# Kernel tuning notes

Measured on AMD Instinct MI355X. Metric: run time of the kernel, lower is better.

## Reference

```python
import jax, jax.numpy as jnp
import numpy as np

N_NODES = 50000
N_EDGES = 800000
IN_DIM = 128
HID_DIM = 128
N_CLASSES = 2


def setup_inputs() -> dict:
    key = jax.random.key(0)
    ks = jax.random.split(key, 8)
    glorot = lambda k, shp: jax.random.normal(k, shp, dtype=jnp.float32) * (2.0 / (shp[0] + shp[1])) ** 0.5
    return {
        "x": jax.random.normal(ks[0], (N_NODES, IN_DIM), dtype=jnp.float32),
        "edge_index": jax.random.randint(ks[1], (2, N_EDGES), 0, N_NODES, dtype=jnp.int64),
        "W1": glorot(ks[2], (IN_DIM, HID_DIM)),
        "b1": jnp.zeros((HID_DIM,), dtype=jnp.float32),
        "W2": glorot(ks[3], (HID_DIM, HID_DIM)),
        "b2": jnp.zeros((HID_DIM,), dtype=jnp.float32),
        "Wc": glorot(ks[4], (HID_DIM, N_CLASSES)),
        "bc": jnp.zeros((N_CLASSES,), dtype=jnp.float32),
    }


def _gcn_norm(edge_index, num_nodes):
    # PyG gcn_norm with self-loops: norm_e = deg[src]^-1/2 * deg[dst]^-1/2
    loop = jnp.arange(num_nodes, dtype=edge_index.dtype)
    src = jnp.concatenate([edge_index[0], loop])
    dst = jnp.concatenate([edge_index[1], loop])
    deg = jax.ops.segment_sum(jnp.ones_like(dst, dtype=jnp.float32), dst,
                              num_segments=num_nodes)
    dis = jnp.where(deg > 0, jax.lax.rsqrt(jnp.maximum(deg, 1.0)), 0.0)
    norm = dis[src] * dis[dst]  # [E + N]
    return src, dst, norm


def _gcn_conv(h, src, dst, norm, W, b, num_nodes):
    h = h @ W                              # [N, out]
    msg = h[src] * norm[:, None]           # gather + scale  [E+N, out]
    out = jax.ops.segment_sum(msg, dst, num_segments=num_nodes)  # scatter-add
    return out + b


def reference(x, edge_index, W1, b1, W2, b2, Wc, bc):
    n = x.shape[0]
    src, dst, norm = _gcn_norm(edge_index, n)
    h = _gcn_conv(x, src, dst, norm, W1, b1, n)
    h = jax.nn.relu(h)  # dropout is identity in eval mode
    h = _gcn_conv(h, src, dst, norm, W2, b2, n)
    return h @ Wc + bc  # [N, num_classes]
```

## Files before the change

### kernel.cpp

```cpp
#include <hip/hip_runtime.h>

static inline size_t align_up(size_t x, size_t a) { return (x + a - 1) & ~(a - 1); }

typedef short bf16x8 __attribute__((ext_vector_type(8)));
typedef float f32x4 __attribute__((ext_vector_type(4)));
typedef int i32x4 __attribute__((ext_vector_type(4)));
typedef float f32x4v __attribute__((ext_vector_type(4)));
typedef unsigned u32x4 __attribute__((ext_vector_type(4)));

#define BK 64
#define SEGE 4096
#define CAP 32
#define PAD 64

__device__ __forceinline__ unsigned bf_rne(float x) {
  unsigned u = __float_as_uint(x);
  return (u + 0x7FFFu + ((u >> 16) & 1u)) >> 16;
}
__device__ __forceinline__ unsigned bf_pack(float lo, float hi) {
  return bf_rne(lo) | (bf_rne(hi) << 16);
}

union BFU { u32x4 u; bf16x8 v; };


__global__ __launch_bounds__(256) void k1_kernel(const int* __restrict__ ei, int E,
                                                 int nseg, int nb,
                                                 unsigned* __restrict__ queue,
                                                 int* __restrict__ hdr,
                                                 const float* __restrict__ W1,
                                                 const float* __restrict__ W2,
                                                 const float* __restrict__ Wc,
                                                 const float* __restrict__ b2,
                                                 const float* __restrict__ bc,
                                                 u32x4* __restrict__ Bpack,
                                                 float* __restrict__ Wf,
                                                 float* __restrict__ bf) {
  __shared__ int lcnt[832];
  __shared__ float sWc[256];
  int t = threadIdx.x;
  int b = blockIdx.x;
  if (b < nseg) {
    for (int i = t; i < nb; i += 256) lcnt[i] = 0;
    __syncthreads();
#pragma unroll
    for (int j = 0; j < SEGE / 1024; ++j) {
      int e = b * SEGE + j * 1024 + t * 4;
      if (e < E) {
        i32x4 s4 = __builtin_nontemporal_load((const i32x4*)(ei + e));
        i32x4 d4 = __builtin_nontemporal_load((const i32x4*)(ei + E + e));
        int ss[4] = {s4.x, s4.y, s4.z, s4.w};
        int dd[4] = {d4.x, d4.y, d4.z, d4.w};
#pragma unroll
        for (int k = 0; k < 4; ++k) {
          int bkt = dd[k] >> 6;
          int off = atomicAdd(&lcnt[bkt], 1);
          if (off < CAP)
            queue[((size_t)bkt * nseg + b) * CAP + off] =
                (unsigned)ss[k] | ((unsigned)(dd[k] & 63) << 16);
        }
      }
    }
    __syncthreads();
    for (int i = t; i < nb; i += 256) hdr[(size_t)b * nb + i] = min(lcnt[i], CAP);
  } else if (b < nseg + 8) {
    int idx = (b - nseg) * 256 + t;
    int l = idx & 63;
    int s = (idx >> 6) & 3;
    int ct = idx >> 8;
    int k0 = s * 32 + (l >> 4) * 8;
    int col = ct * 16 + (l & 15);
    float v[8];
#pragma unroll
    for (int j = 0; j < 8; ++j) v[j] = W1[(size_t)(k0 + j) * 128 + col];
    u32x4 u;
    u.x = bf_pack(v[0], v[1]);
    u.y = bf_pack(v[2], v[3]);
    u.z = bf_pack(v[4], v[5]);
    u.w = bf_pack(v[6], v[7]);
    Bpack[idx] = u;
  } else {
    sWc[t] = Wc[t];
    __syncthreads();
    int i = t >> 1, c = t & 1;
    const float4* row = (const float4*)(W2 + (size_t)i * 128);
    float s = 0.f;
#pragma unroll
    for (int k4 = 0; k4 < 32; ++k4) {
      float4 w = row[k4];
      s = fmaf(w.x, sWc[(k4 * 4 + 0) * 2 + c], s);
      s = fmaf(w.y, sWc[(k4 * 4 + 1) * 2 + c], s);
      s = fmaf(w.z, sWc[(k4 * 4 + 2) * 2 + c], s);
      s = fmaf(w.w, sWc[(k4 * 4 + 3) * 2 + c], s);
    }
    Wf[i * 2 + c] = s;
    if (i == 0) {
      float bb = bc[c];
      for (int k = 0; k < 128; ++k) bb = fmaf(b2[k], sWc[k * 2 + c], bb);
      bf[c] = bb;
    }
  }
}


__global__ __launch_bounds__(256) void k2_kernel(const unsigned* __restrict__ queue,
                                                 const int* __restrict__ hdr,
                                                 int nseg, int nb,
                                                 int* __restrict__ cnt,
                                                 unsigned short* __restrict__ csr_src,
                                                 int n_nodes,
                                                 const float* __restrict__ x,
                                                 const u32x4* __restrict__ Bpack,
                                                 unsigned short* __restrict__ hout,
                                                 int n_rows) {
  __shared__ float sT[4][16][66];
  int t = threadIdx.x;
  if ((int)blockIdx.x < nb) {
    unsigned short* scsr = (unsigned short*)sT;
    int* ccur = (int*)((char*)sT + BK * PAD * 2);
    int* hdrL = ccur + BK;
    int bk = blockIdx.x;
    if (t < BK) ccur[t] = 0;
    if (t < nseg) hdrL[t] = hdr[(size_t)t * nb + bk];
    __syncthreads();
    const unsigned* qbk = queue + (size_t)bk * nseg * CAP;
    int slots = nseg * CAP;
    for (int sl = t; sl < slots; sl += 256) {
      int seg = sl >> 5;
      int off = sl & (CAP - 1);
      if (off < hdrL[seg]) {
        unsigned u = qbk[sl];
        int dl = (u >> 16) & 63;
        int p = atomicAdd(&ccur[dl], 1);
        if (p < PAD) scsr[dl * PAD + p] = (unsigned short)(u & 0xFFFFu);
      }
    }
    __syncthreads();
    uint4* gdst = (uint4*)(csr_src + (size_t)bk * BK * PAD);
    const uint4* lsrc = (const uint4*)scsr;
    gdst[t] = lsrc[t];
    gdst[t + 256] = lsrc[t + 256];
    if (t < BK) {
      int gn = bk * BK + t;
      if (gn < n_nodes) cnt[gn] = min(ccur[t], PAD);
    }
    return;
  }
  int w = t >> 6, l = t & 63;
  int rowbase = ((int)blockIdx.x - nb) * 64 + w * 16;
  int r = l & 15, kg = l >> 4;
  int grow = rowbase + r;
  bool valid = grow < n_rows;
  const float* xr = x + (size_t)grow * 128;

  bf16x8 afrag[4];
#pragma unroll
  for (int s = 0; s < 4; ++s) {
    f32x4v lo = {0.f, 0.f, 0.f, 0.f}, hi = lo;
    if (valid) {
      lo = __builtin_nontemporal_load((const f32x4v*)(xr + s * 32 + kg * 8));
      hi = __builtin_nontemporal_load((const f32x4v*)(xr + s * 32 + kg * 8 + 4));
    }
    BFU bu;
    bu.u.x = bf_pack(lo.x, lo.y);
    bu.u.y = bf_pack(lo.z, lo.w);
    bu.u.z = bf_pack(hi.x, hi.y);
    bu.u.w = bf_pack(hi.z, hi.w);
    afrag[s] = bu.v;
  }

  f32x4 acc[8] = {};
  const u32x4* bp = Bpack + l;
  u32x4 b0[4], b1[4];
#pragma unroll
  for (int s = 0; s < 4; ++s) b0[s] = bp[s * 64];

#define MM_STEP(CT, CUR, NXT)                                                   \
  {                                                                             \
    if (CT < 7) {                                                               \
      _Pragma("unroll") for (int s = 0; s < 4; ++s) NXT[s] =                    \
          bp[((CT + 1) * 4 + s) * 64];                                          \
    }                                                                           \
    _Pragma("unroll") for (int s = 0; s < 4; ++s) {                             \
      BFU bb;                                                                   \
      bb.u = CUR[s];                                                            \
      acc[CT] = __builtin_amdgcn_mfma_f32_16x16x32_bf16(afrag[s], bb.v,         \
                                                        acc[CT], 0, 0, 0);      \
    }                                                                           \
  }
  MM_STEP(0, b0, b1)
  MM_STEP(1, b1, b0)
  MM_STEP(2, b0, b1)
  MM_STEP(3, b1, b0)
  MM_STEP(4, b0, b1)
  MM_STEP(5, b1, b0)
  MM_STEP(6, b0, b1)
  MM_STEP(7, b1, b0)
#undef MM_STEP

  int erow = l >> 2;
  int eseg = l & 3;
  int g2 = rowbase + erow;
#pragma unroll
  for (int hf = 0; hf < 2; ++hf) {
    __syncthreads();
#pragma unroll
    for (int ct = 0; ct < 4; ++ct) {
#pragma unroll
      for (int rg = 0; rg < 4; ++rg)
        sT[w][kg * 4 + rg][ct * 16 + r] = acc[hf * 4 + ct][rg];
    }
    __syncthreads();
    float4 v0 = *(const float4*)&sT[w][erow][eseg * 16 + 0];
    float4 v1 = *(const float4*)&sT[w][erow][eseg * 16 + 4];
    float4 v2 = *(const float4*)&sT[w][erow][eseg * 16 + 8];
    float4 v3 = *(const float4*)&sT[w][erow][eseg * 16 + 12];
    if (g2 < n_rows) {
      u32x4 ua, ub;
      ua.x = bf_pack(v0.x, v0.y);
      ua.y = bf_pack(v0.z, v0.w);
      ua.z = bf_pack(v1.x, v1.y);
      ua.w = bf_pack(v1.z, v1.w);
      ub.x = bf_pack(v2.x, v2.y);
      ub.y = bf_pack(v2.z, v2.w);
      ub.z = bf_pack(v3.x, v3.y);
      ub.w = bf_pack(v3.z, v3.w);
      u32x4* dst = (u32x4*)(hout + (size_t)g2 * 128 + hf * 64 + eseg * 16);
      __builtin_nontemporal_store(ua, dst);
      __builtin_nontemporal_store(ub, dst + 1);
    }
  }
}


__global__ __launch_bounds__(256) void agg1_kernel(const unsigned short* __restrict__ h,
                                                   const unsigned short* __restrict__ csr_src,
                                                   const int* __restrict__ cnt,
                                                   const float* __restrict__ bias,
                                                   const float* __restrict__ Wf,
                                                   float2* __restrict__ g_out,
                                                   int n_nodes) {
  int node = blockIdx.x * 4 + (threadIdx.x >> 6);
  if (node >= n_nodes) return;
  int lane = threadIdx.x & 63;
  int g = lane >> 4;
  int sub = lane & 15;
  int deg = cnt[node];
  if (deg > PAD) deg = PAD;
  float dn = rsqrtf((float)(cnt[node] + 1));
  float a[8] = {};
#define UNPACK_FMA8(u, s)                                                  \
  {                                                                        \
    a[0] = fmaf(s, __uint_as_float((u).x << 16), a[0]);                    \
    a[1] = fmaf(s, __uint_as_float((u).x & 0xFFFF0000u), a[1]);            \
    a[2] = fmaf(s, __uint_as_float((u).y << 16), a[2]);                    \
    a[3] = fmaf(s, __uint_as_float((u).y & 0xFFFF0000u), a[3]);            \
    a[4] = fmaf(s, __uint_as_float((u).z << 16), a[4]);                    \
    a[5] = fmaf(s, __uint_as_float((u).z & 0xFFFF0000u), a[5]);            \
    a[6] = fmaf(s, __uint_as_float((u).w << 16), a[6]);                    \
    a[7] = fmaf(s, __uint_as_float((u).w & 0xFFFF0000u), a[7]);            \
  }
  if (g == 0) {
    uint4 su = ((const uint4*)(h + (size_t)node * 128))[sub];
    UNPACK_FMA8(su, dn);
  }
  const unsigned short* crow = csr_src + (size_t)node * PAD;
  int s_my = 0;
  float w_my = 0.f;
  if (lane < deg) {
    s_my = crow[lane];
    w_my = rsqrtf((float)(cnt[s_my] + 1));
  }
  for (int t0 = 0; t0 < deg; t0 += 16) {
    int t = t0 + g;
    int s0 = __shfl(s_my, t, 64);       float y0 = __shfl(w_my, t, 64);
    int s1 = __shfl(s_my, t + 4, 64);   float y1 = __shfl(w_my, t + 4, 64);
    int s2 = __shfl(s_my, t + 8, 64);   float y2 = __shfl(w_my, t + 8, 64);
    int s3 = __shfl(s_my, t + 12, 64);  float y3 = __shfl(w_my, t + 12, 64);
    uint4 u0 = ((const uint4*)(h + (size_t)s0 * 128))[sub];
    uint4 u1 = ((const uint4*)(h + (size_t)s1 * 128))[sub];
    uint4 u2 = ((const uint4*)(h + (size_t)s2 * 128))[sub];
    uint4 u3 = ((const uint4*)(h + (size_t)s3 * 128))[sub];
    UNPACK_FMA8(u0, y0);
    UNPACK_FMA8(u1, y1);
    UNPACK_FMA8(u2, y2);
    UNPACK_FMA8(u3, y3);
  }
#pragma unroll
  for (int c = 0; c < 8; ++c) {
    a[c] += __shfl_xor(a[c], 16, 64);
    a[c] += __shfl_xor(a[c], 32, 64);
  }
  const float4* b4 = (const float4*)bias;
  float4 bb0 = b4[sub * 2], bb1 = b4[sub * 2 + 1];
  float o[8];
  o[0] = fmaxf(fmaf(a[0], dn, bb0.x), 0.f);
  o[1] = fmaxf(fmaf(a[1], dn, bb0.y), 0.f);
  o[2] = fmaxf(fmaf(a[2], dn, bb0.z), 0.f);
  o[3] = fmaxf(fmaf(a[3], dn, bb0.w), 0.f);
  o[4] = fmaxf(fmaf(a[4], dn, bb1.x), 0.f);
  o[5] = fmaxf(fmaf(a[5], dn, bb1.y), 0.f);
  o[6] = fmaxf(fmaf(a[6], dn, bb1.z), 0.f);
  o[7] = fmaxf(fmaf(a[7], dn, bb1.w), 0.f);
  const float2* wf2 = (const float2*)Wf;
  int kbase = sub * 8;
  float p0 = 0.f, p1 = 0.f;
#pragma unroll
  for (int j = 0; j < 8; ++j) {
    float2 w = wf2[kbase + j];
    p0 = fmaf(o[j], w.x, p0);
    p1 = fmaf(o[j], w.y, p1);
  }
#pragma unroll
  for (int off = 8; off; off >>= 1) {
    p0 += __shfl_xor(p0, off, 64);
    p1 += __shfl_xor(p1, off, 64);
  }
  if (lane == 0) g_out[node] = make_float2(p0, p1);
}


__global__ __launch_bounds__(256) void agg2_kernel(const float2* __restrict__ gin,
                                                   const unsigned short* __restrict__ csr_src,
                                                   const int* __restrict__ cnt,
                                                   const float* __restrict__ bf,
                                                   float2* __restrict__ out, int n_nodes) {
  int tid = threadIdx.x;
  int node = blockIdx.x * 32 + (tid >> 3);
  if (node >= n_nodes) return;
  int sl = tid & 7;
  float dn = rsqrtf((float)(cnt[node] + 1));
  float2 acc = make_float2(0.f, 0.f);
  if (sl == 0) {
    float2 gs = gin[node];
    acc.x = dn * gs.x;
    acc.y = dn * gs.y;
  }
  int deg = cnt[node];
  if (deg > PAD) deg = PAD;
  const unsigned short* crow = csr_src + (size_t)node * PAD;
  for (int e = sl; e < deg; e += 8) {
    int s = crow[e];
    float w = rsqrtf((float)(cnt[s] + 1));
    float2 gv = gin[s];
    acc.x = fmaf(w, gv.x, acc.x);
    acc.y = fmaf(w, gv.y, acc.y);
  }
#pragma unroll
  for (int off = 1; off < 8; off <<= 1) {
    acc.x += __shfl_xor(acc.x, off, 64);
    acc.y += __shfl_xor(acc.y, off, 64);
  }
  if (sl == 0) {
    float2 o;
    o.x = fmaf(acc.x, dn, bf[0]);
    o.y = fmaf(acc.y, dn, bf[1]);
    out[node] = o;
  }
}


extern "C" void kernel_launch(void* const* d_in, const int* in_sizes, int n_in,
                              void* d_out, int out_size, void* d_ws, size_t ws_size,
                              hipStream_t stream) {
  const float* x  = (const float*)d_in[0];
  const int*   ei = (const int*)d_in[1];
  const float* W1 = (const float*)d_in[2];
  const float* b1 = (const float*)d_in[3];
  const float* W2 = (const float*)d_in[4];
  const float* b2 = (const float*)d_in[5];
  const float* Wc = (const float*)d_in[6];
  const float* bc = (const float*)d_in[7];
  float* out = (float*)d_out;

  int N = in_sizes[0] / 128;
  int E = in_sizes[1] / 2;

  int nseg = (E + SEGE - 1) / SEGE;
  int nb   = (N + BK - 1) / BK;

  char* p = (char*)d_ws;
  size_t o = 0;
  auto alloc = [&](size_t bytes) {
    void* r = p + o;
    o = align_up(o + bytes, 256);
    return r;
  };
  unsigned* queue = (unsigned*)alloc((size_t)nb * nseg * CAP * 4);
  int*      hdr   = (int*)alloc((size_t)nseg * nb * 4);
  int*      cnt   = (int*)alloc((size_t)N * 4);
  unsigned short* csr_src = (unsigned short*)alloc((size_t)nb * BK * PAD * 2);
  unsigned short* hBF = (unsigned short*)alloc((size_t)N * 128 * 2);
  float2*   gbuf  = (float2*)alloc((size_t)N * 8);
  u32x4*    Bpack = (u32x4*)alloc(2048 * 16);
  float*    Wf    = (float*)alloc(128 * 2 * 4);
  float*    bf    = (float*)alloc(2 * 4);
  (void)ws_size;

  int nmm = (N + 63) / 64;

  k1_kernel<<<nseg + 9, 256, 0, stream>>>(ei, E, nseg, nb, queue, hdr,
                                          W1, W2, Wc, b2, bc, Bpack, Wf, bf);
  k2_kernel<<<nb + nmm, 256, 0, stream>>>(queue, hdr, nseg, nb, cnt, csr_src, N,
                                          x, Bpack, hBF, N);
  agg1_kernel<<<(N + 3) / 4, 256, 0, stream>>>(hBF, csr_src, cnt, b1, Wf, gbuf, N);
  agg2_kernel<<<(N + 31) / 32, 256, 0, stream>>>(gbuf, csr_src, cnt, (const float*)bf,
                                                 (float2*)out, N);
}
```

Baseline: 80.45 us.

## Split binning into 1024-thread kernel and reorder k2 blocks matmul-first

The weight-prep work moves out of the fused k1 kernel into its own small kprep kernel. Edge binning goes into a separate kbin kernel where each 1024-thread block handles one 4096-edge segment in a single pass instead of four loop iterations of 256 threads. In k2 the block order is swapped so the matmul blocks come first and the CSR-build blocks come last. The goal is more parallelism during binning and better scheduling overlap in k2, at the cost of one extra kernel launch.

```diff
diff --git a/kernel.cpp b/kernel.cpp
--- a/kernel.cpp
+++ b/kernel.cpp
@@ -24,47 +24,19 @@
 union BFU { u32x4 u; bf16x8 v; };
 
 
-__global__ __launch_bounds__(256) void k1_kernel(const int* __restrict__ ei, int E,
-                                                 int nseg, int nb,
-                                                 unsigned* __restrict__ queue,
-                                                 int* __restrict__ hdr,
-                                                 const float* __restrict__ W1,
-                                                 const float* __restrict__ W2,
-                                                 const float* __restrict__ Wc,
-                                                 const float* __restrict__ b2,
-                                                 const float* __restrict__ bc,
-                                                 u32x4* __restrict__ Bpack,
-                                                 float* __restrict__ Wf,
-                                                 float* __restrict__ bf) {
-  __shared__ int lcnt[832];
+__global__ __launch_bounds__(256) void kprep_kernel(const float* __restrict__ W1,
+                                                    const float* __restrict__ W2,
+                                                    const float* __restrict__ Wc,
+                                                    const float* __restrict__ b2,
+                                                    const float* __restrict__ bc,
+                                                    u32x4* __restrict__ Bpack,
+                                                    float* __restrict__ Wf,
+                                                    float* __restrict__ bf) {
   __shared__ float sWc[256];
   int t = threadIdx.x;
   int b = blockIdx.x;
-  if (b < nseg) {
-    for (int i = t; i < nb; i += 256) lcnt[i] = 0;
-    __syncthreads();
-#pragma unroll
-    for (int j = 0; j < SEGE / 1024; ++j) {
-      int e = b * SEGE + j * 1024 + t * 4;
-      if (e < E) {
-        i32x4 s4 = __builtin_nontemporal_load((const i32x4*)(ei + e));
-        i32x4 d4 = __builtin_nontemporal_load((const i32x4*)(ei + E + e));
-        int ss[4] = {s4.x, s4.y, s4.z, s4.w};
-        int dd[4] = {d4.x, d4.y, d4.z, d4.w};
-#pragma unroll
-        for (int k = 0; k < 4; ++k) {
-          int bkt = dd[k] >> 6;
-          int off = atomicAdd(&lcnt[bkt], 1);
-          if (off < CAP)
-            queue[((size_t)bkt * nseg + b) * CAP + off] =
-                (unsigned)ss[k] | ((unsigned)(dd[k] & 63) << 16);
-        }
-      }
-    }
-    __syncthreads();
-    for (int i = t; i < nb; i += 256) hdr[(size_t)b * nb + i] = min(lcnt[i], CAP);
-  } else if (b < nseg + 8) {
-    int idx = (b - nseg) * 256 + t;
+  if (b < 8) {
+    int idx = b * 256 + t;
     int l = idx & 63;
     int s = (idx >> 6) & 3;
     int ct = idx >> 8;
@@ -103,9 +75,38 @@
 }
 
 
+__global__ __launch_bounds__(1024) void kbin_kernel(const int* __restrict__ ei, int E,
+                                                    int nseg, int nb,
+                                                    unsigned* __restrict__ queue,
+                                                    int* __restrict__ hdr) {
+  __shared__ int lcnt[832];
+  int t = threadIdx.x;
+  int b = blockIdx.x;
+  for (int i = t; i < nb; i += 1024) lcnt[i] = 0;
+  __syncthreads();
+  int e = b * SEGE + t * 4;
+  if (e < E) {
+    i32x4 s4 = __builtin_nontemporal_load((const i32x4*)(ei + e));
+    i32x4 d4 = __builtin_nontemporal_load((const i32x4*)(ei + E + e));
+    int ss[4] = {s4.x, s4.y, s4.z, s4.w};
+    int dd[4] = {d4.x, d4.y, d4.z, d4.w};
+#pragma unroll
+    for (int k = 0; k < 4; ++k) {
+      int bkt = dd[k] >> 6;
+      int off = atomicAdd(&lcnt[bkt], 1);
+      if (off < CAP)
+        queue[((size_t)bkt * nseg + b) * CAP + off] =
+            (unsigned)ss[k] | ((unsigned)(dd[k] & 63) << 16);
+    }
+  }
+  __syncthreads();
+  for (int i = t; i < nb; i += 1024) hdr[(size_t)b * nb + i] = min(lcnt[i], CAP);
+}
+
+
 __global__ __launch_bounds__(256) void k2_kernel(const unsigned* __restrict__ queue,
                                                  const int* __restrict__ hdr,
-                                                 int nseg, int nb,
+                                                 int nseg, int nb, int nmm,
                                                  int* __restrict__ cnt,
                                                  unsigned short* __restrict__ csr_src,
                                                  int n_nodes,
@@ -115,11 +116,11 @@
                                                  int n_rows) {
   __shared__ float sT[4][16][66];
   int t = threadIdx.x;
-  if ((int)blockIdx.x < nb) {
+  if ((int)blockIdx.x >= nmm) {
     unsigned short* scsr = (unsigned short*)sT;
     int* ccur = (int*)((char*)sT + BK * PAD * 2);
     int* hdrL = ccur + BK;
-    int bk = blockIdx.x;
+    int bk = (int)blockIdx.x - nmm;
     if (t < BK) ccur[t] = 0;
     if (t < nseg) hdrL[t] = hdr[(size_t)t * nb + bk];
     __syncthreads();
@@ -147,7 +148,7 @@
     return;
   }
   int w = t >> 6, l = t & 63;
-  int rowbase = ((int)blockIdx.x - nb) * 64 + w * 16;
+  int rowbase = (int)blockIdx.x * 64 + w * 16;
   int r = l & 15, kg = l >> 4;
   int grow = rowbase + r;
   bool valid = grow < n_rows;
@@ -399,9 +400,9 @@
 
   int nmm = (N + 63) / 64;
 
-  k1_kernel<<<nseg + 9, 256, 0, stream>>>(ei, E, nseg, nb, queue, hdr,
-                                          W1, W2, Wc, b2, bc, Bpack, Wf, bf);
-  k2_kernel<<<nb + nmm, 256, 0, stream>>>(queue, hdr, nseg, nb, cnt, csr_src, N,
+  kprep_kernel<<<9, 256, 0, stream>>>(W1, W2, Wc, b2, bc, Bpack, Wf, bf);
+  kbin_kernel<<<nseg, 1024, 0, stream>>>(ei, E, nseg, nb, queue, hdr);
+  k2_kernel<<<nmm + nb, 256, 0, stream>>>(queue, hdr, nseg, nb, nmm, cnt, csr_src, N,
                                           x, Bpack, hBF, N);
   agg1_kernel<<<(N + 3) / 4, 256, 0, stream>>>(hBF, csr_src, cnt, b1, Wf, gbuf, N);
   agg2_kernel<<<(N + 31) / 32, 256, 0, stream>>>(gbuf, csr_src, cnt, (const float*)bf,
```

After: 84.90 us, median of 4. 1.06x slower.
